# Performance work log

Hardware: AMD Instinct MI355X
Metric: run time of the kernel (lower is better)

The kernel has to match this reference:

```python
import jax, jax.numpy as jnp
import numpy as np

B, N, S = 8, 4096, 1024
D1, D2 = 128, 256
IN_C = D1 + D2
MLP = [256, 256]
BN_EPS = 1e-5


def setup_inputs() -> dict:
    key = jax.random.key(0)
    ks = jax.random.split(key, 32)
    inp = {
        'xyz1': jax.random.uniform(ks[0], (B, 3, N), dtype=jnp.float32),
        'xyz2': jax.random.uniform(ks[1], (B, 3, S), dtype=jnp.float32),
        'points1': jax.random.normal(ks[2], (B, D1, N), dtype=jnp.float32),
        'points2': jax.random.normal(ks[3], (B, D2, S), dtype=jnp.float32),
        'colors1': jax.random.normal(ks[4], (B, D1, N), dtype=jnp.float32),
        'colors2': jax.random.normal(ks[5], (B, D2, S), dtype=jnp.float32),
    }
    # conv1x1 + BN params for the two MLP stacks (points / colors)
    k = 6
    last = IN_C
    for li, out_c in enumerate(MLP, start=1):
        for tag in ('p', 'c'):
            scale = 1.0 / np.sqrt(last)
            inp[f'W{tag}{li}'] = jax.random.uniform(ks[k], (out_c, last), jnp.float32, -scale, scale); k += 1
            inp[f'b{tag}{li}'] = jax.random.uniform(ks[k], (out_c,), jnp.float32, -scale, scale); k += 1
            inp[f'g{tag}{li}'] = jnp.ones((out_c,), jnp.float32)
            inp[f'be{tag}{li}'] = jnp.zeros((out_c,), jnp.float32)
        last = out_c
    return inp


def _square_distance(src, dst):
    # src [B,N,3], dst [B,S,3] -> [B,N,S]
    d = -2.0 * jnp.einsum('bnc,bsc->bns', src, dst)
    d = d + jnp.sum(src * src, -1)[:, :, None]
    d = d + jnp.sum(dst * dst, -1)[:, None, :]
    return d


def _three_interp(xyz1, xyz2, feat2):
    # xyz1 [B,N,3], xyz2 [B,S,3], feat2 [B,S,D] -> [B,N,D]
    dists = _square_distance(xyz1, xyz2)              # [B,N,S]
    neg_d3, idx = jax.lax.top_k(-dists, 3)            # smallest 3 distances
    d3 = -neg_d3                                      # [B,N,3] ascending
    recip = 1.0 / (d3 + 1e-8)
    weight = recip / jnp.sum(recip, axis=2, keepdims=True)
    gathered = jax.vmap(lambda f, i: f[i])(feat2, idx)  # [B,N,3,D]
    return jnp.sum(gathered * weight[..., None], axis=2)


def _conv_bn_relu(x, W, b, g, be):
    # x [B,N,Cin]; conv1x1 == per-point linear; BN in training mode (batch stats)
    y = jnp.einsum('bnc,oc->bno', x, W) + b
    m = jnp.mean(y, axis=(0, 1))
    v = jnp.var(y, axis=(0, 1))
    yn = (y - m) * jax.lax.rsqrt(v + BN_EPS)
    return jax.nn.relu(yn * g + be)


def reference(xyz1, xyz2, points1, points2, colors1, colors2,
              Wp1, bp1, gp1, bep1, Wc1, bc1, gc1, bec1,
              Wp2, bp2, gp2, bep2, Wc2, bc2, gc2, bec2):
    x1 = jnp.transpose(xyz1, (0, 2, 1))   # [B,N,3]
    x2 = jnp.transpose(xyz2, (0, 2, 1))   # [B,S,3]
    p2 = jnp.transpose(points2, (0, 2, 1))  # [B,S,D2]
    c2 = jnp.transpose(colors2, (0, 2, 1))

    interp_p = _three_interp(x1, x2, p2)  # [B,N,D2]
    interp_c = _three_interp(x1, x2, c2)

    p1 = jnp.transpose(points1, (0, 2, 1))  # [B,N,D1]
    c1 = jnp.transpose(colors1, (0, 2, 1))
    new_p = jnp.concatenate([p1, interp_p], axis=-1)  # [B,N,IN_C]
    new_c = jnp.concatenate([c1, interp_c], axis=-1)

    new_p = _conv_bn_relu(new_p, Wp1, bp1, gp1, bep1)
    new_p = _conv_bn_relu(new_p, Wp2, bp2, gp2, bep2)
    new_c = _conv_bn_relu(new_c, Wc1, bc1, gc1, bec1)
    new_c = _conv_bn_relu(new_c, Wc2, bc2, gc2, bec2)

    return (jnp.transpose(new_p, (0, 2, 1)), jnp.transpose(new_c, (0, 2, 1)))
```

## Files before the change

kernel.cpp:

```cpp
#include <hip/hip_runtime.h>
#include <cstdint>
#include <cstddef>


#define B_   8
#define N_   4096
#define S_   1024
#define D1_  128
#define D2_  256
#define INC_ 384
#define OC_  256
#define M_   (B_ * N_)

typedef __attribute__((ext_vector_type(8))) short sh8;
typedef __attribute__((ext_vector_type(4))) float f32x4;
typedef __attribute__((ext_vector_type(4))) unsigned short ush4;
typedef __attribute__((ext_vector_type(8))) unsigned short ush8;

__device__ __forceinline__ unsigned short bf16rne(float f) {
    union { float f; unsigned u; } v; v.f = f;
    return (unsigned short)((v.u + 0x7FFFu + ((v.u >> 16) & 1u)) >> 16);
}
__device__ __forceinline__ float bf2f(unsigned short h) {
    union { unsigned u; float f; } v; v.u = ((unsigned)h) << 16;
    return v.f;
}
__device__ __forceinline__ void gload16(const void* gsrc, void* lds) {
    __builtin_amdgcn_global_load_lds(
        (const __attribute__((address_space(1))) void*)gsrc,
        (__attribute__((address_space(3))) void*)lds, 16, 0, 0);
}

__global__ __launch_bounds__(256) void transpose2b_kernel(
    const float* __restrict__ src, unsigned short* __restrict__ dst)
{
    __shared__ float tile[32][33];
    const float* s = src + (size_t)blockIdx.z * D2_ * S_;
    unsigned short* d = dst + (size_t)blockIdx.z * S_ * D2_;
    int c = blockIdx.x * 32 + threadIdx.x;
#pragma unroll
    for (int i = 0; i < 4; ++i) {
        int r = blockIdx.y * 32 + threadIdx.y + i * 8;
        tile[threadIdx.y + i * 8][threadIdx.x] = s[(size_t)r * S_ + c];
    }
    __syncthreads();
    int r2 = blockIdx.y * 32 + threadIdx.x;
#pragma unroll
    for (int i = 0; i < 4; ++i) {
        int c2 = blockIdx.x * 32 + threadIdx.y + i * 8;
        d[(size_t)c2 * D2_ + r2] = bf16rne(tile[threadIdx.x][threadIdx.y + i * 8]);
    }
}

__global__ __launch_bounds__(256) void convw_kernel(
    const float* __restrict__ Wp1, const float* __restrict__ Wc1,
    const float* __restrict__ Wp2, const float* __restrict__ Wc2,
    unsigned short* __restrict__ Wb1, unsigned short* __restrict__ Wb2)
{
    int e = (blockIdx.x * 256 + threadIdx.x) * 4;
    const float* src; unsigned short* dst; int off;
    if (e < 98304)       { src = Wp1; dst = Wb1;          off = e; }
    else if (e < 196608) { src = Wc1; dst = Wb1 + 98304;  off = e - 98304; }
    else if (e < 262144) { src = Wp2; dst = Wb2;          off = e - 196608; }
    else                 { src = Wc2; dst = Wb2 + 65536;  off = e - 262144; }
    float4 v = *(const float4*)(src + off);
    ush4 o; o[0] = bf16rne(v.x); o[1] = bf16rne(v.y); o[2] = bf16rne(v.z); o[3] = bf16rne(v.w);
    *(ush4*)(dst + off) = o;
}

#define INS(pd, pi) { \
    bool l0 = (pd < d0) || (pd == d0 && pi < i0); \
    bool l1 = (pd < d1) || (pd == d1 && pi < i1); \
    bool l2 = (pd < d2) || (pd == d2 && pi < i2); \
    d2 = l1 ? d1 : (l2 ? pd : d2);  i2 = l1 ? i1 : (l2 ? pi : i2); \
    d1 = l0 ? d0 : (l1 ? pd : d1);  i1 = l0 ? i0 : (l1 ? pi : i1); \
    d0 = l0 ? pd : d0;              i0 = l0 ? pi : i0; \
}

__global__ __launch_bounds__(256) void top3_kernel(
    const float* __restrict__ xyz1, const float* __restrict__ xyz2,
    int* __restrict__ idxo, float* __restrict__ wo)
{
    __shared__ float4 sc[S_];
    const int b = blockIdx.y;
    const int tid = threadIdx.x;
    const float* x2 = xyz2 + (size_t)b * 3 * S_;
    for (int s = tid; s < S_; s += 256) {
        float xs = x2[s], ys = x2[S_ + s], zs = x2[2 * S_ + s];
        sc[s] = make_float4(xs, ys, zs, xs * xs + ys * ys + zs * zs);
    }
    __syncthreads();
    const int q = blockIdx.x * 32 + (tid >> 3);
    const int sub = tid & 7;
    const float* x1 = xyz1 + (size_t)b * 3 * N_;
    const float xq = x1[q], yq = x1[N_ + q], zq = x1[2 * N_ + q];
    const float n1 = xq * xq + yq * yq + zq * zq;
    float d0 = 3.4e38f, d1 = 3.4e38f, d2 = 3.4e38f;
    int i0 = 0, i1 = 0, i2 = 0;
#pragma unroll 4
    for (int j = 0; j < 128; ++j) {
        int s = j * 8 + sub;
        float4 v = sc[s];
        float dot = xq * v.x + yq * v.y + zq * v.z;
        float d = (n1 - 2.0f * dot) + v.w;
        bool c0 = d < d0, c1 = d < d1, c2 = d < d2;
        d2 = c1 ? d1 : (c2 ? d : d2); i2 = c1 ? i1 : (c2 ? s : i2);
        d1 = c0 ? d0 : (c1 ? d : d1); i1 = c0 ? i0 : (c1 ? s : i1);
        d0 = c0 ? d : d0;             i0 = c0 ? s : i0;
    }
#pragma unroll
    for (int off = 1; off < 8; off <<= 1) {
        float pd0 = __shfl_xor(d0, off), pd1 = __shfl_xor(d1, off), pd2 = __shfl_xor(d2, off);
        int   pi0 = __shfl_xor(i0, off), pi1 = __shfl_xor(i1, off), pi2 = __shfl_xor(i2, off);
        INS(pd0, pi0) INS(pd1, pi1) INS(pd2, pi2)
    }
    if (sub == 0) {
        float r0 = 1.f / (d0 + 1e-8f);
        float r1 = 1.f / (d1 + 1e-8f);
        float r2 = 1.f / (d2 + 1e-8f);
        float rs = r0 + r1 + r2;
        int base = (b * N_ + q) * 3;
        idxo[base] = i0; idxo[base + 1] = i1; idxo[base + 2] = i2;
        wo[base] = r0 / rs; wo[base + 1] = r1 / rs; wo[base + 2] = r2 / rs;
    }
}

__global__ __launch_bounds__(256) void buildxA_kernel(
    const float* __restrict__ points1, const float* __restrict__ colors1,
    unsigned short* __restrict__ Xp)
{
    const int t = blockIdx.z, b = blockIdx.y, n0 = blockIdx.x * 64;
    const float* x1 = t ? colors1 : points1;
    const int tid = threadIdx.x;
    __shared__ float tileA[64][132];

#pragma unroll
    for (int it = 0; it < 8; ++it) {
        int fl4 = it * 256 + tid;
        int d = fl4 >> 4, nl = (fl4 & 15) * 4;
        float4 v = *(const float4*)(x1 + ((size_t)b * D1_ + d) * N_ + n0 + nl);
        tileA[nl][d] = v.x; tileA[nl + 1][d] = v.y; tileA[nl + 2][d] = v.z; tileA[nl + 3][d] = v.w;
    }
    __syncthreads();
    size_t mbase = (size_t)t * M_ + (size_t)b * N_ + n0;
#pragma unroll
    for (int it = 0; it < 4; ++it) {
        int e8 = it * 256 + tid;
        int r = e8 >> 4, dc = (e8 & 15) * 8;
        ush8 o;
#pragma unroll
        for (int j = 0; j < 8; ++j) o[j] = bf16rne(tileA[r][dc + j]);
        *(ush8*)(Xp + (mbase + r) * D1_ + dc) = o;
    }
}

__global__ __launch_bounds__(512, 2) void gemm1f_kernel(
    const unsigned short* __restrict__ Xp,
    const unsigned short* __restrict__ p2b,
    const unsigned short* __restrict__ c2b,
    const int* __restrict__ idxw, const float* __restrict__ wgtw,
    const unsigned short* __restrict__ Wb1,
    unsigned short* __restrict__ Y1,
    float* __restrict__ psum, float* __restrict__ psq)
{
    const int t  = blockIdx.y;
    const int m0 = blockIdx.x * 256;
    const int bb = m0 >> 12;
    const unsigned short* Aw  = Wb1 + (size_t)t * (OC_ * INC_);
    const unsigned short* Xb  = Xp + (size_t)t * M_ * D1_;
    const unsigned short* f2b = t ? c2b : p2b;

    __shared__ __align__(16) char smem[131072];

    const int tid  = threadIdx.x;
    const int lane = tid & 63;
    const int wid  = tid >> 6;
    const int wc   = wid & 3;
    const int wm   = wid >> 2;
    const int srow = tid >> 3;
    const int k8   = (tid & 7) * 8;
    const int sk   = ((tid & 7) ^ (srow & 7)) * 8;
    const int kgrp = (lane >> 4) * 16;

    int gi[4][3]; float gw[4][3];
#pragma unroll
    for (int p = 0; p < 4; ++p) {
        int base = (m0 + p * 64 + srow) * 3;
#pragma unroll
        for (int j = 0; j < 3; ++j) { gi[p][j] = idxw[base + j]; gw[p][j] = wgtw[base + j]; }
    }

    f32x4 acc[4][8];
#pragma unroll
    for (int i = 0; i < 4; ++i)
#pragma unroll
        for (int j = 0; j < 8; ++j) acc[i][j] = f32x4{0.f, 0.f, 0.f, 0.f};

    auto stageA = [&](int buf, int kc) {
#pragma unroll
        for (int p = 0; p < 4; ++p)
            gload16(Aw + (size_t)(p * 64 + srow) * INC_ + kc + sk,
                    smem + buf * 32768 + p * 8192 + wid * 1024);
    };
    auto stageBX = [&](int buf, int kc) {
#pragma unroll
        for (int p = 0; p < 4; ++p)
            gload16(Xb + (size_t)(m0 + p * 64 + srow) * D1_ + kc + sk,
                    smem + 65536 + buf * 32768 + p * 8192 + wid * 1024);
    };
    auto stageBG = [&](int buf, int kc) {
        const int d0k = kc - D1_ + k8;
#pragma unroll
        for (int p = 0; p < 4; ++p) {
            int row = p * 64 + srow;
            ush8 a0 = *(const ush8*)(f2b + ((size_t)bb * S_ + gi[p][0]) * D2_ + d0k);
            ush8 a1 = *(const ush8*)(f2b + ((size_t)bb * S_ + gi[p][1]) * D2_ + d0k);
            ush8 a2 = *(const ush8*)(f2b + ((size_t)bb * S_ + gi[p][2]) * D2_ + d0k);
            ush8 ov;
#pragma unroll
            for (int j = 0; j < 8; ++j)
                ov[j] = bf16rne(gw[p][0] * bf2f(a0[j]) + gw[p][1] * bf2f(a1[j])
                              + gw[p][2] * bf2f(a2[j]));
            *(ush8*)(smem + 65536 + buf * 32768 + row * 128
                     + ((k8 * 2) ^ ((row & 7) << 4))) = ov;
        }
    };
    auto compute = [&](int buf) {
#pragma unroll
        for (int kk = 0; kk < 2; ++kk) {
            sh8 a[4], b[8];
#pragma unroll
            for (int f = 0; f < 4; ++f) {
                int ra = wc * 64 + (lane & 15) + f * 16;
                a[f] = *(const sh8*)(smem + buf * 32768 + ra * 128
                        + ((kk * 64 + kgrp) ^ ((ra & 7) << 4)));
            }
#pragma unroll
            for (int f = 0; f < 8; ++f) {
                int rb = wm * 128 + (lane & 15) + f * 16;
                b[f] = *(const sh8*)(smem + 65536 + buf * 32768 + rb * 128
                        + ((kk * 64 + kgrp) ^ ((rb & 7) << 4)));
            }
#pragma unroll
            for (int fc = 0; fc < 4; ++fc)
#pragma unroll
                for (int fm = 0; fm < 8; ++fm)
                    acc[fc][fm] = __builtin_amdgcn_mfma_f32_16x16x32_bf16(
                        a[fc], b[fm], acc[fc][fm], 0, 0, 0);
        }
    };

    stageA(0, 0); stageBX(0, 0);
    __syncthreads();
    int cur = 0;
    for (int step = 0; step < 6; ++step) {
        int kcn = (step + 1) * 64;
        if (step < 5) {
            stageA(cur ^ 1, kcn);
            if (kcn < D1_) stageBX(cur ^ 1, kcn);
            else           stageBG(cur ^ 1, kcn);
        }
        compute(cur);
        __syncthreads();
        cur ^= 1;
    }

    const int mrow = m0 + wm * 128 + (lane & 15);
    const int chq  = (lane >> 4) * 4;
#pragma unroll
    for (int fm = 0; fm < 8; ++fm)
#pragma unroll
        for (int fc = 0; fc < 4; ++fc) {
            ush4 v;
#pragma unroll
            for (int r = 0; r < 4; ++r) v[r] = bf16rne(acc[fc][fm][r]);
            *(ush4*)(Y1 + ((size_t)t * M_ + mrow + fm * 16) * OC_
                      + wc * 64 + fc * 16 + chq) = v;
        }

    float* sArr = (float*)smem;
    const int contrib = wm * 16 + (lane & 15);
#pragma unroll
    for (int ph = 0; ph < 2; ++ph) {
#pragma unroll
        for (int fc = 0; fc < 4; ++fc) {
            f32x4 s4;
#pragma unroll
            for (int r = 0; r < 4; ++r) {
                float s = 0.f;
#pragma unroll
                for (int fm = 0; fm < 8; ++fm) { float v = acc[fc][fm][r]; s += ph ? v * v : v; }
                s4[r] = s;
            }
            *(f32x4*)&sArr[contrib * 264 + wc * 64 + fc * 16 + chq] = s4;
        }
        __syncthreads();
        if (tid < 256) {
            float s = 0.f;
#pragma unroll
            for (int k = 0; k < 32; ++k) s += sArr[((k + tid) & 31) * 264 + tid];
            (ph ? psq : psum)[((size_t)t * 128 + blockIdx.x) * 256 + tid] = s;
        }
        __syncthreads();
    }
}

__global__ __launch_bounds__(256) void reduce_kernel(
    const float* __restrict__ psum, const float* __restrict__ psq,
    const float* __restrict__ gp, const float* __restrict__ bep,
    const float* __restrict__ gc, const float* __restrict__ bec,
    float* __restrict__ ss, int layerOff)
{
    const int t = blockIdx.x, cs = blockIdx.y;
    const int tid = threadIdx.x;
    const int cl = tid & 63, grp = tid >> 6;
    const int c = cs * 64 + cl;
    float s = 0.f, q = 0.f;
    for (int k = grp; k < 128; k += 4) {
        s += psum[((size_t)t * 128 + k) * 256 + c];
        q += psq [((size_t)t * 128 + k) * 256 + c];
    }
    __shared__ float ls[4][64], lq[4][64];
    ls[grp][cl] = s; lq[grp][cl] = q;
    __syncthreads();
    if (tid < 64) {
        s = ls[0][cl] + ls[1][cl] + ls[2][cl] + ls[3][cl];
        q = lq[0][cl] + lq[1][cl] + lq[2][cl] + lq[3][cl];
        float mean = s * (1.f / (float)M_);
        float var  = q * (1.f / (float)M_) - mean * mean;
        float inv  = rsqrtf(var + 1e-5f);
        float g = (t ? gc : gp)[c], be = (t ? bec : bep)[c];
        float sc = g * inv;
        ss[layerOff + t * 256 + c]       = sc;
        ss[layerOff + 512 + t * 256 + c] = be - mean * sc;
    }
}

__global__ __launch_bounds__(512, 2) void gemm2f_kernel(
    const unsigned short* __restrict__ Y1,
    const unsigned short* __restrict__ Wb2,
    const float* __restrict__ ss,
    unsigned short* __restrict__ y2b,
    float* __restrict__ psum, float* __restrict__ psq)
{
    const int t  = blockIdx.y;
    const int m0 = blockIdx.x * 256;
    const unsigned short* Aw = Wb2 + (size_t)t * (OC_ * OC_);
    const unsigned short* By = Y1 + (size_t)t * M_ * OC_;

    __shared__ __align__(16) char smem[131072];
    __shared__ float Slds[256], Hlds[256];

    const int tid  = threadIdx.x;
    const int lane = tid & 63;
    const int wid  = tid >> 6;
    const int wc   = wid & 3;
    const int wm   = wid >> 2;
    const int srow = tid >> 3;
    const int k8   = (tid & 7) * 8;
    const int sk   = ((tid & 7) ^ (srow & 7)) * 8;
    const int kgrp = (lane >> 4) * 16;

    if (tid < 256) { Slds[tid] = ss[t * 256 + tid]; Hlds[tid] = ss[512 + t * 256 + tid]; }
    __syncthreads();

    f32x4 acc[4][8];
#pragma unroll
    for (int i = 0; i < 4; ++i)
#pragma unroll
        for (int j = 0; j < 8; ++j) acc[i][j] = f32x4{0.f, 0.f, 0.f, 0.f};

    auto stageA = [&](int buf, int kc) {
#pragma unroll
        for (int p = 0; p < 4; ++p)
            gload16(Aw + (size_t)(p * 64 + srow) * OC_ + kc + sk,
                    smem + buf * 32768 + p * 8192 + wid * 1024);
    };
    auto stageBY = [&](int buf, int kc) {
#pragma unroll
        for (int p = 0; p < 4; ++p) {
            int row = p * 64 + srow;
            ush8 yv = *(const ush8*)(By + (size_t)(m0 + row) * OC_ + kc + k8);
            ush8 ov;
#pragma unroll
            for (int j = 0; j < 8; ++j) {
                float y = bf2f(yv[j]);
                ov[j] = bf16rne(fmaxf(0.f, fmaf(y, Slds[kc + k8 + j], Hlds[kc + k8 + j])));
            }
            *(ush8*)(smem + 65536 + buf * 32768 + row * 128
                     + ((k8 * 2) ^ ((row & 7) << 4))) = ov;
        }
    };
    auto compute = [&](int buf) {
#pragma unroll
        for (int kk = 0; kk < 2; ++kk) {
            sh8 a[4], b[8];
#pragma unroll
            for (int f = 0; f < 4; ++f) {
                int ra = wc * 64 + (lane & 15) + f * 16;
                a[f] = *(const sh8*)(smem + buf * 32768 + ra * 128
                        + ((kk * 64 + kgrp) ^ ((ra & 7) << 4)));
            }
#pragma unroll
            for (int f = 0; f < 8; ++f) {
                int rb = wm * 128 + (lane & 15) + f * 16;
                b[f] = *(const sh8*)(smem + 65536 + buf * 32768 + rb * 128
                        + ((kk * 64 + kgrp) ^ ((rb & 7) << 4)));
            }
#pragma unroll
            for (int fc = 0; fc < 4; ++fc)
#pragma unroll
                for (int fm = 0; fm < 8; ++fm)
                    acc[fc][fm] = __builtin_amdgcn_mfma_f32_16x16x32_bf16(
                        a[fc], b[fm], acc[fc][fm], 0, 0, 0);
        }
    };

    stageA(0, 0); stageBY(0, 0);
    __syncthreads();
    int cur = 0;
    for (int step = 0; step < 4; ++step) {
        int kcn = (step + 1) * 64;
        if (step < 3) { stageA(cur ^ 1, kcn); stageBY(cur ^ 1, kcn); }
        compute(cur);
        __syncthreads();
        cur ^= 1;
    }

    const int mrow = m0 + wm * 128 + (lane & 15);
    const int chq  = (lane >> 4) * 4;
#pragma unroll
    for (int fm = 0; fm < 8; ++fm)
#pragma unroll
        for (int fc = 0; fc < 4; ++fc) {
            ush4 v;
#pragma unroll
            for (int r = 0; r < 4; ++r) v[r] = bf16rne(acc[fc][fm][r]);
            *(ush4*)(y2b + ((size_t)t * M_ + mrow + fm * 16) * OC_
                      + wc * 64 + fc * 16 + chq) = v;
        }

    float* sArr = (float*)smem;
    const int contrib = wm * 16 + (lane & 15);
#pragma unroll
    for (int ph = 0; ph < 2; ++ph) {
#pragma unroll
        for (int fc = 0; fc < 4; ++fc) {
            f32x4 s4;
#pragma unroll
            for (int r = 0; r < 4; ++r) {
                float s = 0.f;
#pragma unroll
                for (int fm = 0; fm < 8; ++fm) { float v = acc[fc][fm][r]; s += ph ? v * v : v; }
                s4[r] = s;
            }
            *(f32x4*)&sArr[contrib * 264 + wc * 64 + fc * 16 + chq] = s4;
        }
        __syncthreads();
        if (tid < 256) {
            float s = 0.f;
#pragma unroll
            for (int k = 0; k < 32; ++k) s += sArr[((k + tid) & 31) * 264 + tid];
            (ph ? psq : psum)[((size_t)t * 128 + blockIdx.x) * 256 + tid] = s;
        }
        __syncthreads();
    }
}

__global__ __launch_bounds__(256) void bnT_kernel(
    const unsigned short* __restrict__ y2b, const float* __restrict__ ss,
    float* __restrict__ out)
{
    const int z = blockIdx.z;
    const int t = z >> 3, b = z & 7;
    const int o0 = blockIdx.y * 64;
    const int n0 = blockIdx.x * 64;
    const int tid = threadIdx.x;
    __shared__ unsigned short tile[64][72];

    const unsigned short* src = y2b + ((size_t)t * M_ + (size_t)b * N_ + n0) * OC_ + o0;
#pragma unroll
    for (int it = 0; it < 2; ++it) {
        int u = it * 256 + tid;
        int m_l = u >> 3, o8 = (u & 7) * 8;
        *(ush8*)&tile[m_l][o8] = *(const ush8*)(src + (size_t)m_l * OC_ + o8);
    }
    __syncthreads();
#pragma unroll
    for (int it = 0; it < 4; ++it) {
        int v = it * 256 + tid;
        int o_l = v >> 4, n4 = (v & 15) * 4;
        int o = o0 + o_l;
        float sc = ss[1024 + t * 256 + o];
        float sh = ss[1536 + t * 256 + o];
        float4 w;
        w.x = fmaxf(0.f, fmaf(bf2f(tile[n4][o_l]),     sc, sh));
        w.y = fmaxf(0.f, fmaf(bf2f(tile[n4 + 1][o_l]), sc, sh));
        w.z = fmaxf(0.f, fmaf(bf2f(tile[n4 + 2][o_l]), sc, sh));
        w.w = fmaxf(0.f, fmaf(bf2f(tile[n4 + 3][o_l]), sc, sh));
        *(float4*)(out + (((size_t)t * B_ + b) * OC_ + o) * N_ + n0 + n4) = w;
    }
}

extern "C" void kernel_launch(void* const* d_in, const int* in_sizes, int n_in,
                              void* d_out, int out_size, void* d_ws, size_t ws_size,
                              hipStream_t stream)
{
    const float* xyz1    = (const float*)d_in[0];
    const float* xyz2    = (const float*)d_in[1];
    const float* points1 = (const float*)d_in[2];
    const float* points2 = (const float*)d_in[3];
    const float* colors1 = (const float*)d_in[4];
    const float* colors2 = (const float*)d_in[5];
    const float* Wp1  = (const float*)d_in[6];
    const float* gp1  = (const float*)d_in[8];
    const float* bep1 = (const float*)d_in[9];
    const float* Wc1  = (const float*)d_in[10];
    const float* gc1  = (const float*)d_in[12];
    const float* bec1 = (const float*)d_in[13];
    const float* Wp2  = (const float*)d_in[14];
    const float* gp2  = (const float*)d_in[16];
    const float* bep2 = (const float*)d_in[17];
    const float* Wc2  = (const float*)d_in[18];
    const float* gc2  = (const float*)d_in[20];
    const float* bec2 = (const float*)d_in[21];

    char* ws = (char*)d_ws;
    unsigned short* y2b  = (unsigned short*)(ws + 0);
    unsigned short* Xp   = (unsigned short*)(ws + 0);
    unsigned short* p2b  = (unsigned short*)(ws + 16777216);
    unsigned short* c2b  = (unsigned short*)(ws + 20971520);
    int*   idxw = (int*)  (ws + 25165824);
    float* wgtw = (float*)(ws + 25559040);
    unsigned short* Y1   = (unsigned short*)(ws + 33554432);
    unsigned short* Wb1  = (unsigned short*)(ws + 67108864);
    unsigned short* Wb2  = (unsigned short*)(ws + 67895296);
    float* psum = (float*)(ws + 68419584);
    float* psq  = (float*)(ws + 68681728);
    float* ssb  = (float*)(ws + 68943872);
    float* out  = (float*)d_out;

    dim3 tb(32, 8);
    transpose2b_kernel<<<dim3(32, 8, 8), tb, 0, stream>>>(points2, p2b);
    transpose2b_kernel<<<dim3(32, 8, 8), tb, 0, stream>>>(colors2, c2b);
    convw_kernel<<<320, 256, 0, stream>>>(Wp1, Wc1, Wp2, Wc2, Wb1, Wb2);
    top3_kernel<<<dim3(128, 8), 256, 0, stream>>>(xyz1, xyz2, idxw, wgtw);
    buildxA_kernel<<<dim3(64, 8, 2), 256, 0, stream>>>(points1, colors1, Xp);
    gemm1f_kernel<<<dim3(128, 2), 512, 0, stream>>>(Xp, p2b, c2b, idxw, wgtw,
                                                    Wb1, Y1, psum, psq);
    reduce_kernel<<<dim3(2, 4), 256, 0, stream>>>(psum, psq, gp1, bep1, gc1, bec1, ssb, 0);
    gemm2f_kernel<<<dim3(128, 2), 512, 0, stream>>>(Y1, Wb2, ssb, y2b, psum, psq);
    reduce_kernel<<<dim3(2, 4), 256, 0, stream>>>(psum, psq, gp2, bep2, gc2, bec2, ssb, 1024);
    bnT_kernel<<<dim3(64, 4, 16), 256, 0, stream>>>(y2b, ssb, out);
}
```

Before: 133.2 us.

## Fuse five preprocessing kernels into one launch and remap gemm1 blocks per XCD

Folds the two feature transposes, the weight conversion, the top-3 neighbour search and the points1/colors1 transpose into a single front_kernel that dispatches work by block-index range, with one shared-memory buffer sized for the largest branch. This removes four kernel launches and lets the independent preprocessing phases run concurrently. The gemm1 grid is flattened and block IDs are remapped so blocks landing on the same XCD share a tensor type and a contiguous row range, aiming for better L2 reuse of the gathered features and weights. The cost is a larger shared-memory allocation for every block and divergent branch code in one kernel, which may lower occupancy for the lighter branches.

```diff
diff --git a/kernel.cpp b/kernel.cpp
--- a/kernel.cpp
+++ b/kernel.cpp
@@ -31,43 +31,6 @@
         (__attribute__((address_space(3))) void*)lds, 16, 0, 0);
 }
 
-__global__ __launch_bounds__(256) void transpose2b_kernel(
-    const float* __restrict__ src, unsigned short* __restrict__ dst)
-{
-    __shared__ float tile[32][33];
-    const float* s = src + (size_t)blockIdx.z * D2_ * S_;
-    unsigned short* d = dst + (size_t)blockIdx.z * S_ * D2_;
-    int c = blockIdx.x * 32 + threadIdx.x;
-#pragma unroll
-    for (int i = 0; i < 4; ++i) {
-        int r = blockIdx.y * 32 + threadIdx.y + i * 8;
-        tile[threadIdx.y + i * 8][threadIdx.x] = s[(size_t)r * S_ + c];
-    }
-    __syncthreads();
-    int r2 = blockIdx.y * 32 + threadIdx.x;
-#pragma unroll
-    for (int i = 0; i < 4; ++i) {
-        int c2 = blockIdx.x * 32 + threadIdx.y + i * 8;
-        d[(size_t)c2 * D2_ + r2] = bf16rne(tile[threadIdx.x][threadIdx.y + i * 8]);
-    }
-}
-
-__global__ __launch_bounds__(256) void convw_kernel(
-    const float* __restrict__ Wp1, const float* __restrict__ Wc1,
-    const float* __restrict__ Wp2, const float* __restrict__ Wc2,
-    unsigned short* __restrict__ Wb1, unsigned short* __restrict__ Wb2)
-{
-    int e = (blockIdx.x * 256 + threadIdx.x) * 4;
-    const float* src; unsigned short* dst; int off;
-    if (e < 98304)       { src = Wp1; dst = Wb1;          off = e; }
-    else if (e < 196608) { src = Wc1; dst = Wb1 + 98304;  off = e - 98304; }
-    else if (e < 262144) { src = Wp2; dst = Wb2;          off = e - 196608; }
-    else                 { src = Wc2; dst = Wb2 + 65536;  off = e - 262144; }
-    float4 v = *(const float4*)(src + off);
-    ush4 o; o[0] = bf16rne(v.x); o[1] = bf16rne(v.y); o[2] = bf16rne(v.z); o[3] = bf16rne(v.w);
-    *(ush4*)(dst + off) = o;
-}
-
 #define INS(pd, pi) { \
     bool l0 = (pd < d0) || (pd == d0 && pi < i0); \
     bool l1 = (pd < d1) || (pd == d1 && pi < i1); \
@@ -77,80 +40,116 @@
     d0 = l0 ? pd : d0;              i0 = l0 ? pi : i0; \
 }
 
-__global__ __launch_bounds__(256) void top3_kernel(
+__global__ __launch_bounds__(256) void front_kernel(
     const float* __restrict__ xyz1, const float* __restrict__ xyz2,
-    int* __restrict__ idxo, float* __restrict__ wo)
-{
-    __shared__ float4 sc[S_];
-    const int b = blockIdx.y;
-    const int tid = threadIdx.x;
-    const float* x2 = xyz2 + (size_t)b * 3 * S_;
-    for (int s = tid; s < S_; s += 256) {
-        float xs = x2[s], ys = x2[S_ + s], zs = x2[2 * S_ + s];
-        sc[s] = make_float4(xs, ys, zs, xs * xs + ys * ys + zs * zs);
-    }
-    __syncthreads();
-    const int q = blockIdx.x * 32 + (tid >> 3);
-    const int sub = tid & 7;
-    const float* x1 = xyz1 + (size_t)b * 3 * N_;
-    const float xq = x1[q], yq = x1[N_ + q], zq = x1[2 * N_ + q];
-    const float n1 = xq * xq + yq * yq + zq * zq;
-    float d0 = 3.4e38f, d1 = 3.4e38f, d2 = 3.4e38f;
-    int i0 = 0, i1 = 0, i2 = 0;
-#pragma unroll 4
-    for (int j = 0; j < 128; ++j) {
-        int s = j * 8 + sub;
-        float4 v = sc[s];
-        float dot = xq * v.x + yq * v.y + zq * v.z;
-        float d = (n1 - 2.0f * dot) + v.w;
-        bool c0 = d < d0, c1 = d < d1, c2 = d < d2;
-        d2 = c1 ? d1 : (c2 ? d : d2); i2 = c1 ? i1 : (c2 ? s : i2);
-        d1 = c0 ? d0 : (c1 ? d : d1); i1 = c0 ? i0 : (c1 ? s : i1);
-        d0 = c0 ? d : d0;             i0 = c0 ? s : i0;
-    }
-#pragma unroll
-    for (int off = 1; off < 8; off <<= 1) {
-        float pd0 = __shfl_xor(d0, off), pd1 = __shfl_xor(d1, off), pd2 = __shfl_xor(d2, off);
-        int   pi0 = __shfl_xor(i0, off), pi1 = __shfl_xor(i1, off), pi2 = __shfl_xor(i2, off);
-        INS(pd0, pi0) INS(pd1, pi1) INS(pd2, pi2)
-    }
-    if (sub == 0) {
-        float r0 = 1.f / (d0 + 1e-8f);
-        float r1 = 1.f / (d1 + 1e-8f);
-        float r2 = 1.f / (d2 + 1e-8f);
-        float rs = r0 + r1 + r2;
-        int base = (b * N_ + q) * 3;
-        idxo[base] = i0; idxo[base + 1] = i1; idxo[base + 2] = i2;
-        wo[base] = r0 / rs; wo[base + 1] = r1 / rs; wo[base + 2] = r2 / rs;
-    }
-}
-
-__global__ __launch_bounds__(256) void buildxA_kernel(
     const float* __restrict__ points1, const float* __restrict__ colors1,
+    const float* __restrict__ points2, const float* __restrict__ colors2,
+    const float* __restrict__ Wp1, const float* __restrict__ Wc1,
+    const float* __restrict__ Wp2, const float* __restrict__ Wc2,
+    int* __restrict__ idxo, float* __restrict__ wo,
+    unsigned short* __restrict__ p2b, unsigned short* __restrict__ c2b,
+    unsigned short* __restrict__ Wb1, unsigned short* __restrict__ Wb2,
     unsigned short* __restrict__ Xp)
 {
-    const int t = blockIdx.z, b = blockIdx.y, n0 = blockIdx.x * 64;
-    const float* x1 = t ? colors1 : points1;
+    __shared__ __align__(16) char fsm[33792];
+    const int bid = blockIdx.x;
     const int tid = threadIdx.x;
-    __shared__ float tileA[64][132];
-
-#pragma unroll
-    for (int it = 0; it < 8; ++it) {
-        int fl4 = it * 256 + tid;
-        int d = fl4 >> 4, nl = (fl4 & 15) * 4;
-        float4 v = *(const float4*)(x1 + ((size_t)b * D1_ + d) * N_ + n0 + nl);
-        tileA[nl][d] = v.x; tileA[nl + 1][d] = v.y; tileA[nl + 2][d] = v.z; tileA[nl + 3][d] = v.w;
-    }
-    __syncthreads();
-    size_t mbase = (size_t)t * M_ + (size_t)b * N_ + n0;
-#pragma unroll
-    for (int it = 0; it < 4; ++it) {
-        int e8 = it * 256 + tid;
-        int r = e8 >> 4, dc = (e8 & 15) * 8;
-        ush8 o;
-#pragma unroll
-        for (int j = 0; j < 8; ++j) o[j] = bf16rne(tileA[r][dc + j]);
-        *(ush8*)(Xp + (mbase + r) * D1_ + dc) = o;
+
+    if (bid < 1024) {
+        float4* sc = (float4*)fsm;
+        const int b = bid >> 7, qb = bid & 127;
+        const float* x2 = xyz2 + (size_t)b * 3 * S_;
+        for (int s = tid; s < S_; s += 256) {
+            float xs = x2[s], ys = x2[S_ + s], zs = x2[2 * S_ + s];
+            sc[s] = make_float4(xs, ys, zs, xs * xs + ys * ys + zs * zs);
+        }
+        __syncthreads();
+        const int q = qb * 32 + (tid >> 3);
+        const int sub = tid & 7;
+        const float* x1 = xyz1 + (size_t)b * 3 * N_;
+        const float xq = x1[q], yq = x1[N_ + q], zq = x1[2 * N_ + q];
+        const float n1 = xq * xq + yq * yq + zq * zq;
+        float d0 = 3.4e38f, d1 = 3.4e38f, d2 = 3.4e38f;
+        int i0 = 0, i1 = 0, i2 = 0;
+#pragma unroll 4
+        for (int j = 0; j < 128; ++j) {
+            int s = j * 8 + sub;
+            float4 v = sc[s];
+            float dot = xq * v.x + yq * v.y + zq * v.z;
+            float d = (n1 - 2.0f * dot) + v.w;
+            bool c0 = d < d0, c1 = d < d1, c2 = d < d2;
+            d2 = c1 ? d1 : (c2 ? d : d2); i2 = c1 ? i1 : (c2 ? s : i2);
+            d1 = c0 ? d0 : (c1 ? d : d1); i1 = c0 ? i0 : (c1 ? s : i1);
+            d0 = c0 ? d : d0;             i0 = c0 ? s : i0;
+        }
+#pragma unroll
+        for (int off = 1; off < 8; off <<= 1) {
+            float pd0 = __shfl_xor(d0, off), pd1 = __shfl_xor(d1, off), pd2 = __shfl_xor(d2, off);
+            int   pi0 = __shfl_xor(i0, off), pi1 = __shfl_xor(i1, off), pi2 = __shfl_xor(i2, off);
+            INS(pd0, pi0) INS(pd1, pi1) INS(pd2, pi2)
+        }
+        if (sub == 0) {
+            float r0 = 1.f / (d0 + 1e-8f);
+            float r1 = 1.f / (d1 + 1e-8f);
+            float r2 = 1.f / (d2 + 1e-8f);
+            float rs = r0 + r1 + r2;
+            int base = (b * N_ + q) * 3;
+            idxo[base] = i0; idxo[base + 1] = i1; idxo[base + 2] = i2;
+            wo[base] = r0 / rs; wo[base + 1] = r1 / rs; wo[base + 2] = r2 / rs;
+        }
+    } else if (bid < 5120) {
+        float (*tile)[33] = (float(*)[33])fsm;
+        const int u = bid - 1024;
+        const int which = u >> 11;
+        const int v = u & 2047;
+        const int z = v >> 8, rem = v & 255;
+        const int cx = rem & 31, ry = rem >> 5;
+        const int tx = tid & 31, ty = tid >> 5;
+        const float* s = (which ? colors2 : points2) + (size_t)z * D2_ * S_;
+        unsigned short* d = (which ? c2b : p2b) + (size_t)z * S_ * D2_;
+#pragma unroll
+        for (int i = 0; i < 4; ++i)
+            tile[ty + i * 8][tx] = s[(size_t)(ry * 32 + ty + i * 8) * S_ + cx * 32 + tx];
+        __syncthreads();
+#pragma unroll
+        for (int i = 0; i < 4; ++i)
+            d[(size_t)(cx * 32 + ty + i * 8) * D2_ + ry * 32 + tx] =
+                bf16rne(tile[tx][ty + i * 8]);
+    } else if (bid < 5440) {
+        int e = ((bid - 5120) * 256 + tid) * 4;
+        const float* src; unsigned short* dst; int off;
+        if (e < 98304)       { src = Wp1; dst = Wb1;          off = e; }
+        else if (e < 196608) { src = Wc1; dst = Wb1 + 98304;  off = e - 98304; }
+        else if (e < 262144) { src = Wp2; dst = Wb2;          off = e - 196608; }
+        else                 { src = Wc2; dst = Wb2 + 65536;  off = e - 262144; }
+        float4 v = *(const float4*)(src + off);
+        ush4 o; o[0] = bf16rne(v.x); o[1] = bf16rne(v.y); o[2] = bf16rne(v.z); o[3] = bf16rne(v.w);
+        *(ush4*)(dst + off) = o;
+    } else {
+        float (*tileA)[132] = (float(*)[132])fsm;
+        const int u = bid - 5440;
+        const int t = u >> 9, rem = u & 511;
+        const int b = rem >> 6, n0 = (rem & 63) * 64;
+        const float* x1 = t ? colors1 : points1;
+#pragma unroll
+        for (int it = 0; it < 8; ++it) {
+            int fl4 = it * 256 + tid;
+            int d = fl4 >> 4, nl = (fl4 & 15) * 4;
+            float4 v = *(const float4*)(x1 + ((size_t)b * D1_ + d) * N_ + n0 + nl);
+            tileA[nl][d] = v.x; tileA[nl + 1][d] = v.y;
+            tileA[nl + 2][d] = v.z; tileA[nl + 3][d] = v.w;
+        }
+        __syncthreads();
+        size_t mbase = (size_t)t * M_ + (size_t)b * N_ + n0;
+#pragma unroll
+        for (int it = 0; it < 4; ++it) {
+            int e8 = it * 256 + tid;
+            int r = e8 >> 4, dc = (e8 & 15) * 8;
+            ush8 o;
+#pragma unroll
+            for (int j = 0; j < 8; ++j) o[j] = bf16rne(tileA[r][dc + j]);
+            *(ush8*)(Xp + (mbase + r) * D1_ + dc) = o;
+        }
     }
 }
 
@@ -163,9 +162,12 @@
     unsigned short* __restrict__ Y1,
     float* __restrict__ psum, float* __restrict__ psq)
 {
-    const int t  = blockIdx.y;
-    const int m0 = blockIdx.x * 256;
-    const int bb = m0 >> 12;
+    const int wg  = blockIdx.x;
+    const int xcd = wg & 7;
+    const int t   = xcd & 1;
+    const int mt  = (xcd >> 1) * 32 + (wg >> 3);
+    const int m0  = mt * 256;
+    const int bb  = m0 >> 12;
     const unsigned short* Aw  = Wb1 + (size_t)t * (OC_ * INC_);
     const unsigned short* Xb  = Xp + (size_t)t * M_ * D1_;
     const unsigned short* f2b = t ? c2b : p2b;
@@ -299,7 +301,7 @@
             float s = 0.f;
 #pragma unroll
             for (int k = 0; k < 32; ++k) s += sArr[((k + tid) & 31) * 264 + tid];
-            (ph ? psq : psum)[((size_t)t * 128 + blockIdx.x) * 256 + tid] = s;
+            (ph ? psq : psum)[((size_t)t * 128 + mt) * 256 + tid] = s;
         }
         __syncthreads();
     }
@@ -540,14 +542,11 @@
     float* ssb  = (float*)(ws + 68943872);
     float* out  = (float*)d_out;
 
-    dim3 tb(32, 8);
-    transpose2b_kernel<<<dim3(32, 8, 8), tb, 0, stream>>>(points2, p2b);
-    transpose2b_kernel<<<dim3(32, 8, 8), tb, 0, stream>>>(colors2, c2b);
-    convw_kernel<<<320, 256, 0, stream>>>(Wp1, Wc1, Wp2, Wc2, Wb1, Wb2);
-    top3_kernel<<<dim3(128, 8), 256, 0, stream>>>(xyz1, xyz2, idxw, wgtw);
-    buildxA_kernel<<<dim3(64, 8, 2), 256, 0, stream>>>(points1, colors1, Xp);
-    gemm1f_kernel<<<dim3(128, 2), 512, 0, stream>>>(Xp, p2b, c2b, idxw, wgtw,
-                                                    Wb1, Y1, psum, psq);
+    front_kernel<<<6464, 256, 0, stream>>>(xyz1, xyz2, points1, colors1,
+                                           points2, colors2, Wp1, Wc1, Wp2, Wc2,
+                                           idxw, wgtw, p2b, c2b, Wb1, Wb2, Xp);
+    gemm1f_kernel<<<256, 512, 0, stream>>>(Xp, p2b, c2b, idxw, wgtw,
+                                           Wb1, Y1, psum, psq);
     reduce_kernel<<<dim3(2, 4), 256, 0, stream>>>(psum, psq, gp1, bep1, gc1, bec1, ssb, 0);
     gemm2f_kernel<<<dim3(128, 2), 512, 0, stream>>>(Y1, Wb2, ssb, y2b, psum, psq);
     reduce_kernel<<<dim3(2, 4), 256, 0, stream>>>(psum, psq, gp2, bep2, gc2, bec2, ssb, 1024);
```

Result: faster. 119.2 us (-10.6%).
